# Kernel tuning notes

Hardware: AMD Instinct MI355X
Metric: run time of the kernel (lower is better)

Reference implementation:

```python
import jax, jax.numpy as jnp
import numpy as np

L, P, D, AL = 48, 2048, 50, 5
ONEHOT = 5 * D + 5  # 255, leaf one-hot size per encode()


def setup_inputs() -> dict:
    rng = np.random.default_rng(0)
    # node types: 0=leaf 1=unary 2=exist 3=univ 4=binary 5=functor 6=predicate
    node_type = np.zeros((L, P), np.int64)
    node_type[1:] = rng.integers(0, 7, size=(L - 1, P))
    children = -np.ones((L, P, AL), np.int64)
    for l in range(1, L):
        hi = l * P  # children must come from earlier levels (topological order)
        nt = node_type[l]
        n_child = np.where(nt == 0, 0,
                  np.where(nt <= 3, 1,
                  np.where(nt == 4, 2, rng.integers(1, AL + 1, size=P))))
        samp = rng.integers(0, hi, size=(P, AL))
        m = np.arange(AL)[None, :] < n_child[:, None]
        children[l] = np.where(m, samp, -1)
    # two-hot leaf encoding per encode(): v[category]=1 (0..4) and v[i+5]=1
    cat = rng.integers(0, 5, size=(L, P))
    ident = rng.integers(0, 5 * D, size=(L, P))
    onehot = np.zeros((L, P, ONEHOT), np.float32)
    li, pi = np.meshgrid(np.arange(L), np.arange(P), indexing='ij')
    onehot[li, pi, ident + 5] = 1.0
    onehot[li, pi, cat] = 1.0

    def lin(i, out_d, in_d):
        k = jax.random.fold_in(jax.random.key(0), i)
        kw, kb = jax.random.split(k)
        W = jax.random.normal(kw, (out_d, in_d), jnp.float32) * (in_d ** -0.5)
        b = jax.random.normal(kb, (out_d,), jnp.float32) * 0.01
        return W, b

    W_leaf, b_leaf = lin(0, D, ONEHOT)
    W_unary, b_unary = lin(1, D, D)
    W_exist, b_exist = lin(2, D, D)
    W_univ, b_univ = lin(3, D, D)
    W_bin, b_bin = lin(4, D, 3 * D)
    W_fun, b_fun = lin(5, D, (1 + AL) * D)
    W_pred, b_pred = lin(6, D, (1 + AL) * D)
    W_final, b_final = lin(7, ONEHOT, D)
    return dict(node_type=jnp.asarray(node_type, jnp.int32),
                children=jnp.asarray(children, jnp.int32),
                onehot=jnp.asarray(onehot),
                W_leaf=W_leaf, b_leaf=b_leaf, W_unary=W_unary, b_unary=b_unary,
                W_exist=W_exist, b_exist=b_exist, W_univ=W_univ, b_univ=b_univ,
                W_bin=W_bin, b_bin=b_bin, W_fun=W_fun, b_fun=b_fun,
                W_pred=W_pred, b_pred=b_pred, W_final=W_final, b_final=b_final)


def reference(node_type, children, onehot,
              W_leaf, b_leaf, W_unary, b_unary, W_exist, b_exist,
              W_univ, b_univ, W_bin, b_bin, W_fun, b_fun,
              W_pred, b_pred, W_final, b_final):
    relu = jax.nn.relu

    def step(buf, xs):
        l, nt, ch, oh = xs  # nt:[P], ch:[P,AL], oh:[P,ONEHOT]
        leaf = relu(oh @ W_leaf.T + b_leaf)                      # relu(leaf_net(onehot))
        mask = (ch >= 0).astype(buf.dtype)[..., None]
        ce = buf[jnp.clip(ch, 0)] * mask                          # [P,AL,D] child embeddings
        c0, c1 = ce[:, 0], ce[:, 1]
        unary = relu(c0 @ W_unary.T + b_unary)
        exist = relu(c0 @ W_exist.T + b_exist)
        univ = relu(c0 @ W_univ.T + b_univ)
        binv = relu(jnp.concatenate([c0, leaf, c1], -1) @ W_bin.T + b_bin)  # cat[left, op, right]
        fin = jnp.concatenate([leaf, ce.reshape(P, AL * D)], -1)  # [P,(1+AL)*D]
        fun = relu(fin @ W_fun.T + b_fun)
        pred = relu(fin @ W_pred.T + b_pred)
        outs = jnp.stack([leaf, unary, exist, univ, binv, fun, pred])  # [7,P,D]
        out = jnp.take_along_axis(outs, nt[None, :, None], axis=0)[0]
        buf = jax.lax.dynamic_update_slice(buf, out, (l * P, 0))
        return buf, None

    buf0 = jnp.zeros((L * P, D), onehot.dtype)
    xs = (jnp.arange(L), node_type, children, onehot)
    buf, _ = jax.lax.scan(step, buf0, xs)
    root = buf[-1]
    return root @ W_final.T + b_final  # self.final(self.visit(input)), shape [255]
```

## Files before the change

### kernel.cpp

```cpp
#include <hip/hip_runtime.h>

#define L_ 48
#define P_ 2048
#define D_ 50
#define AL_ 5
#define OH_ 255
#define NNODES (L_*P_)
#define MAXN_ 256
#define HSZ 1024
#define NTHREADS 512
#define NWAVES 8

__device__ __forceinline__ float dot50(const float* __restrict__ W, const float* in) {
    float a0 = 0.f, a1 = 0.f, a2 = 0.f, a3 = 0.f;
    #pragma unroll
    for (int j = 0; j < 48; j += 4) {
        float2 w0 = *reinterpret_cast<const float2*>(W + j);
        float2 w1 = *reinterpret_cast<const float2*>(W + j + 2);
        a0 += w0.x * in[j];
        a1 += w0.y * in[j + 1];
        a2 += w1.x * in[j + 2];
        a3 += w1.y * in[j + 3];
    }
    float2 wl = *reinterpret_cast<const float2*>(W + 48);
    a0 += wl.x * in[48];
    a1 += wl.y * in[49];
    return (a0 + a1) + (a2 + a3);
}

__device__ __forceinline__ float dotrow(const float* __restrict__ W, const float* in, int len) {
    float a0 = 0.f, a1 = 0.f, a2 = 0.f, a3 = 0.f;
    int j = 0;
    for (; j + 4 <= len; j += 4) {
        a0 += W[j] * in[j]; a1 += W[j+1] * in[j+1];
        a2 += W[j+2] * in[j+2]; a3 += W[j+3] * in[j+3];
    }
    for (; j < len; ++j) a0 += W[j] * in[j];
    return (a0 + a1) + (a2 + a3);
}

__device__ __forceinline__ float pf4(const float* __restrict__ p, int n, int t, int nth) {
    float s = 0.f;
    for (int i = t * 4; i + 3 < n; i += nth * 4) {
        float4 v = *reinterpret_cast<const float4*>(p + i);
        s += v.x + v.y + v.z + v.w;
    }
    return s;
}

__global__ __launch_bounds__(NTHREADS)
void formula_kernel(const int* __restrict__ node_type,
                    const int* __restrict__ children,
                    const float* __restrict__ onehot,
                    const float* __restrict__ W_leaf,  const float* __restrict__ b_leaf,
                    const float* __restrict__ W_unary, const float* __restrict__ b_unary,
                    const float* __restrict__ W_exist, const float* __restrict__ b_exist,
                    const float* __restrict__ W_univ,  const float* __restrict__ b_univ,
                    const float* __restrict__ W_bin,   const float* __restrict__ b_bin,
                    const float* __restrict__ W_fun,   const float* __restrict__ b_fun,
                    const float* __restrict__ W_pred,  const float* __restrict__ b_pred,
                    const float* __restrict__ W_final, const float* __restrict__ b_final,
                    float* __restrict__ out)
{
    __shared__ int h_key[HSZ];
    __shared__ int h_val[HSZ];
    __shared__ int list[MAXN_];
    __shared__ int nt_l[MAXN_];
    __shared__ int dep[MAXN_];
    __shared__ int order[MAXN_];
    __shared__ int ch_l[MAXN_][AL_];
    __shared__ int dcnt[48], doff[48], dfill[48];
    __shared__ int cnt_sh, maxd_sh;
    __shared__ float emb_s[MAXN_][D_];
    __shared__ float leaf_s[MAXN_][D_];
    __shared__ int   nzj[NWAVES][16];
    __shared__ float nzv[NWAVES][16];

    const int tid  = threadIdx.x;
    const int lane = tid & 63;
    const int wave = tid >> 6;
    volatile int* vcnt = &cnt_sh;

    if (wave == 0) {
        for (int i = lane; i < HSZ; i += 64) h_key[i] = -1;
        __builtin_amdgcn_wave_barrier();
        if (lane == 0) {
            cnt_sh = 1;
            list[0] = NNODES - 1;
            unsigned h = ((unsigned)(NNODES - 1) * 2654435761u) >> 16;
            for (;;) { int i = (int)(h & (HSZ - 1));
                       if (h_key[i] == -1) { h_key[i] = NNODES - 1; h_val[i] = 0; break; } ++h; }
        }
        __builtin_amdgcn_wave_barrier();

        int fs = 0, fe = 1;
        for (int round = 0; round < 48 && fs < fe; ++round) {
            const int npairs = (fe - fs) * AL_;
            for (int base = 0; base < npairs; base += 256) {
                const int m = (npairs - base < 256) ? (npairs - base) : 256;
                int cv[4];
                #pragma unroll
                for (int u = 0; u < 4; ++u) {
                    int t = base + lane + u * 64;
                    cv[u] = (t < base + m)
                        ? children[(size_t)list[fs + t / AL_] * AL_ + (t % AL_)] : -1;
                }
                #pragma unroll
                for (int u = 0; u < 4; ++u) {
                    int c = cv[u];
                    if (c >= 0) {
                        unsigned h = ((unsigned)c * 2654435761u) >> 16;
                        for (;;) {
                            int i = (int)(h & (HSZ - 1));
                            int prev = atomicCAS(&h_key[i], -1, c);
                            if (prev == -1) {
                                int pos = atomicAdd(&cnt_sh, 1);
                                h_val[i] = pos;
                                if (pos < MAXN_) list[pos] = c;
                                break;
                            }
                            if (prev == c) break;
                            ++h;
                        }
                    }
                }
            }
            __builtin_amdgcn_wave_barrier();
            fs = fe;
            int c2 = *vcnt;
            fe = c2 < MAXN_ ? c2 : MAXN_;
            __builtin_amdgcn_wave_barrier();
        }

        const int count = (*vcnt < MAXN_) ? *vcnt : MAXN_;

        for (int t = lane; t < count * 6; t += 64) {
            int i = t / 6, j = t % 6;
            int n = list[i];
            if (j == 0) {
                nt_l[i] = node_type[n];
            } else {
                int c = children[(size_t)n * AL_ + (j - 1)];
                int sl = -1;
                if (c >= 0) {
                    unsigned h = ((unsigned)c * 2654435761u) >> 16;
                    for (;;) {
                        int ii = (int)(h & (HSZ - 1));
                        if (h_key[ii] == c) { sl = h_val[ii]; break; }
                        ++h;
                    }
                    if (sl >= MAXN_) sl = -1;
                }
                ch_l[i][j - 1] = sl;
            }
        }
    } else {
        const int t = tid - 64, nth = NTHREADS - 64;
        float s = 0.f;
        s += pf4(W_leaf,  D_ * OH_,    t, nth);
        s += pf4(W_unary, D_ * D_,     t, nth);
        s += pf4(W_exist, D_ * D_,     t, nth);
        s += pf4(W_univ,  D_ * D_,     t, nth);
        s += pf4(W_bin,   D_ * 3 * D_, t, nth);
        s += pf4(W_fun,   D_ * 6 * D_, t, nth);
        s += pf4(W_pred,  D_ * 6 * D_, t, nth);
        s += pf4(W_final, OH_ * D_,    t, nth);
        if (t < 64) {
            s += b_leaf[t % D_] + b_unary[t % D_] + b_exist[t % D_] + b_univ[t % D_]
               + b_bin[t % D_] + b_fun[t % D_] + b_pred[t % D_] + b_final[t];
        }
        asm volatile("" :: "v"(s));
    }
    __syncthreads();

    const int count = (cnt_sh < MAXN_) ? cnt_sh : MAXN_;

    if (wave == 0) {
        volatile int* vdep = dep;
        for (int i = lane; i < count; i += 64) vdep[i] = 0;
        __builtin_amdgcn_wave_barrier();
        for (int it = 0; it < 48; ++it) {
            bool anych = false;
            for (int i = lane; i < count; i += 64) {
                int d = 0;
                #pragma unroll
                for (int k = 0; k < AL_; ++k) {
                    int cs = ch_l[i][k];
                    if (cs >= 0) { int dd = vdep[cs] + 1; if (dd > d) d = dd; }
                }
                if (d > vdep[i]) { vdep[i] = d; anych = true; }
            }
            __builtin_amdgcn_wave_barrier();
            if (!__any(anych)) break;
        }
        for (int i = lane; i < 48; i += 64) { dcnt[i] = 0; dfill[i] = 0; }
        __builtin_amdgcn_wave_barrier();
        for (int i = lane; i < count; i += 64) atomicAdd(&dcnt[dep[i]], 1);
        __builtin_amdgcn_wave_barrier();
        {
            int v = (lane < 48) ? dcnt[lane] : 0;
            int incl = v;
            #pragma unroll
            for (int dlt = 1; dlt < 64; dlt <<= 1) {
                int o = __shfl_up(incl, dlt);
                if (lane >= dlt) incl += o;
            }
            if (lane < 48) doff[lane] = incl - v;
            unsigned long long b = __ballot(lane < 48 && v != 0);
            if (lane == 0) maxd_sh = 63 - __builtin_clzll(b);
        }
        __builtin_amdgcn_wave_barrier();
        for (int i = lane; i < count; i += 64) {
            int d = dep[i];
            int pos = doff[d] + atomicAdd(&dfill[d], 1);
            order[pos] = i;
        }
    } else {
        for (int slot = wave - 1; slot < count; slot += NWAVES - 1) {
            const int nt = nt_l[slot];
            if (nt >= 1 && nt <= 3) continue;
            const int n = list[slot];
            const float* oh = onehot + (size_t)n * OH_;
            float v[4]; int c2 = 0;
            #pragma unroll
            for (int t = 0; t < 4; ++t) {
                int j = lane * 4 + t;
                v[t] = (j < OH_) ? oh[j] : 0.0f;
                if (v[t] != 0.0f) c2++;
            }
            int incl = c2;
            #pragma unroll
            for (int dlt = 1; dlt < 64; dlt <<= 1) {
                int o = __shfl_up(incl, dlt);
                if (lane >= dlt) incl += o;
            }
            const int excl = incl - c2;
            const int total = __shfl(incl, 63);
            if (total <= 16) {
                int pos = excl;
                #pragma unroll
                for (int t = 0; t < 4; ++t)
                    if (v[t] != 0.0f) { nzj[wave][pos] = lane * 4 + t; nzv[wave][pos] = v[t]; pos++; }
            }
            __builtin_amdgcn_wave_barrier();
            if (lane < D_) {
                float sacc = b_leaf[lane];
                if (total <= 16) {
                    for (int i2 = 0; i2 < total; ++i2)
                        sacc += nzv[wave][i2] * W_leaf[lane * OH_ + nzj[wave][i2]];
                } else {
                    sacc += dotrow(W_leaf + lane * OH_, oh, OH_);
                }
                float lv = fmaxf(sacc, 0.0f);
                if (nt == 0) emb_s[slot][lane] = lv;
                else         leaf_s[slot][lane] = lv;
            }
            __builtin_amdgcn_wave_barrier();
        }
    }
    __syncthreads();

    const int maxd = maxd_sh;

    for (int d = 1; d <= maxd; ++d) {
        const int s0 = doff[d], cn = dcnt[d];
        for (int jj = wave; jj < cn; jj += NWAVES) {
            const int slot = order[s0 + jj];
            const int nt = nt_l[slot];
            if (lane < D_) {
                float s;
                if (nt <= 3) {
                    const float* W = (nt == 1) ? W_unary : (nt == 2) ? W_exist : W_univ;
                    const float* b = (nt == 1) ? b_unary : (nt == 2) ? b_exist : b_univ;
                    s = b[lane];
                    const int cs0 = ch_l[slot][0];
                    if (cs0 >= 0) s += dot50(W + lane * D_, emb_s[cs0]);
                } else if (nt == 4) {
                    const float* W = W_bin + lane * 3 * D_;
                    s = b_bin[lane];
                    const int cs0 = ch_l[slot][0], cs1 = ch_l[slot][1];
                    if (cs0 >= 0) s += dot50(W, emb_s[cs0]);
                    s += dot50(W + D_, leaf_s[slot]);
                    if (cs1 >= 0) s += dot50(W + 2 * D_, emb_s[cs1]);
                } else {
                    const float* W = ((nt == 5) ? W_fun : W_pred) + lane * 6 * D_;
                    s = ((nt == 5) ? b_fun : b_pred)[lane] + dot50(W, leaf_s[slot]);
                    #pragma unroll
                    for (int k = 0; k < AL_; ++k) {
                        int cs = ch_l[slot][k];
                        if (cs >= 0) s += dot50(W + (1 + k) * D_, emb_s[cs]);
                    }
                }
                emb_s[slot][lane] = fmaxf(s, 0.0f);
            }
        }
        __syncthreads();
    }

    for (int o = tid; o < OH_; o += NTHREADS)
        out[o] = b_final[o] + dot50(W_final + o * D_, emb_s[0]);
}

extern "C" void kernel_launch(void* const* d_in, const int* in_sizes, int n_in,
                              void* d_out, int out_size, void* d_ws, size_t ws_size,
                              hipStream_t stream) {
    const int*   node_type = (const int*)d_in[0];
    const int*   children  = (const int*)d_in[1];
    const float* onehot    = (const float*)d_in[2];
    const float* W_leaf  = (const float*)d_in[3];  const float* b_leaf  = (const float*)d_in[4];
    const float* W_unary = (const float*)d_in[5];  const float* b_unary = (const float*)d_in[6];
    const float* W_exist = (const float*)d_in[7];  const float* b_exist = (const float*)d_in[8];
    const float* W_univ  = (const float*)d_in[9];  const float* b_univ  = (const float*)d_in[10];
    const float* W_bin   = (const float*)d_in[11]; const float* b_bin   = (const float*)d_in[12];
    const float* W_fun   = (const float*)d_in[13]; const float* b_fun   = (const float*)d_in[14];
    const float* W_pred  = (const float*)d_in[15]; const float* b_pred  = (const float*)d_in[16];
    const float* W_final = (const float*)d_in[17]; const float* b_final = (const float*)d_in[18];

    float* out = (float*)d_out;

    formula_kernel<<<1, NTHREADS, 0, stream>>>(
        node_type, children, onehot,
        W_leaf, b_leaf, W_unary, b_unary, W_exist, b_exist, W_univ, b_univ,
        W_bin, b_bin, W_fun, b_fun, W_pred, b_pred, W_final, b_final,
        out);
}
```

Baseline: 23.40 us.

## Replace depth-level barriers with ready-flag dataflow over index-sorted nodes

Drops the per-depth dependency computation and level-by-level __syncthreads schedule. Nodes are instead sorted by global index, which is already a topological order, and waves spin on per-node LDS ready flags before consuming child embeddings. The change also prefetches each discovered node's children, type and onehot rows into LDS scratch during BFS, fuses the leaf computation into the main loop, and pads embedding rows for float4 LDS reads. The spin-waiting adds a risk of stalls and depends on fence ordering, and the rank sort is quadratic in the node count.

```diff
diff --git a/kernel.cpp b/kernel.cpp
--- a/kernel.cpp
+++ b/kernel.cpp
@@ -10,21 +10,29 @@
 #define HSZ 1024
 #define NTHREADS 512
 #define NWAVES 8
-
-__device__ __forceinline__ float dot50(const float* __restrict__ W, const float* in) {
+#define SPIN_BOUND (1 << 24)
+
+__device__ __forceinline__ void pfl(const void* g, void* lds_scratch) {
+    __builtin_amdgcn_global_load_lds(
+        (const __attribute__((address_space(1))) unsigned int*)g,
+        (__attribute__((address_space(3))) unsigned int*)lds_scratch,
+        4, 0, 0);
+}
+
+__device__ __forceinline__ float dot50L(const float* __restrict__ Wg, const float* inL) {
+    const float4* x4 = (const float4*)inL;
     float a0 = 0.f, a1 = 0.f, a2 = 0.f, a3 = 0.f;
     #pragma unroll
-    for (int j = 0; j < 48; j += 4) {
-        float2 w0 = *reinterpret_cast<const float2*>(W + j);
-        float2 w1 = *reinterpret_cast<const float2*>(W + j + 2);
-        a0 += w0.x * in[j];
-        a1 += w0.y * in[j + 1];
-        a2 += w1.x * in[j + 2];
-        a3 += w1.y * in[j + 3];
-    }
-    float2 wl = *reinterpret_cast<const float2*>(W + 48);
-    a0 += wl.x * in[48];
-    a1 += wl.y * in[49];
+    for (int q = 0; q < 12; ++q) {
+        float4 x = x4[q];
+        float2 w0 = *(const float2*)(Wg + q * 4);
+        float2 w1 = *(const float2*)(Wg + q * 4 + 2);
+        a0 += w0.x * x.x; a1 += w0.y * x.y;
+        a2 += w1.x * x.z; a3 += w1.y * x.w;
+    }
+    float4 xt = x4[12];
+    float2 wt = *(const float2*)(Wg + 48);
+    a0 += wt.x * xt.x; a1 += wt.y * xt.y;
     return (a0 + a1) + (a2 + a3);
 }
 
@@ -66,36 +74,43 @@
     __shared__ int h_val[HSZ];
     __shared__ int list[MAXN_];
     __shared__ int nt_l[MAXN_];
-    __shared__ int dep[MAXN_];
     __shared__ int order[MAXN_];
+    __shared__ int rdy[MAXN_];
     __shared__ int ch_l[MAXN_][AL_];
-    __shared__ int dcnt[48], doff[48], dfill[48];
-    __shared__ int cnt_sh, maxd_sh;
-    __shared__ float emb_s[MAXN_][D_];
-    __shared__ float leaf_s[MAXN_][D_];
+    __shared__ int cnt_sh;
+    __shared__ __align__(16) float emb_s[MAXN_][52];
+    __shared__ __align__(16) float lrow[NWAVES][52];
     __shared__ int   nzj[NWAVES][16];
     __shared__ float nzv[NWAVES][16];
+    __shared__ unsigned pfscr[64];
 
     const int tid  = threadIdx.x;
     const int lane = tid & 63;
     const int wave = tid >> 6;
-    volatile int* vcnt = &cnt_sh;
 
     if (wave == 0) {
         for (int i = lane; i < HSZ; i += 64) h_key[i] = -1;
         __builtin_amdgcn_wave_barrier();
         if (lane == 0) {
             cnt_sh = 1;
-            list[0] = NNODES - 1;
-            unsigned h = ((unsigned)(NNODES - 1) * 2654435761u) >> 16;
+            const int root = NNODES - 1;
+            list[0] = root;
+            unsigned h = ((unsigned)root * 2654435761u) >> 16;
             for (;;) { int i = (int)(h & (HSZ - 1));
-                       if (h_key[i] == -1) { h_key[i] = NNODES - 1; h_val[i] = 0; break; } ++h; }
+                       if (h_key[i] == -1) { h_key[i] = root; h_val[i] = 0; break; } ++h; }
+            pfl(&node_type[root], pfscr);
+            const char* ohb = (const char*)(onehot + (size_t)root * OH_);
+            #pragma unroll
+            for (int q = 0; q < 16; ++q) pfl(ohb + q * 64, pfscr);
+            pfl(ohb + 1016, pfscr);
         }
         __builtin_amdgcn_wave_barrier();
 
+        int total_reg = 1;
         int fs = 0, fe = 1;
         for (int round = 0; round < 48 && fs < fe; ++round) {
             const int npairs = (fe - fs) * AL_;
+            int ic = 0;
             for (int base = 0; base < npairs; base += 256) {
                 const int m = (npairs - base < 256) ? (npairs - base) : 256;
                 int cv[4];
@@ -117,6 +132,14 @@
                                 int pos = atomicAdd(&cnt_sh, 1);
                                 h_val[i] = pos;
                                 if (pos < MAXN_) list[pos] = c;
+                                ic++;
+                                const char* chb = (const char*)&children[(size_t)c * AL_];
+                                pfl(chb, pfscr); pfl(chb + 16, pfscr);
+                                pfl(&node_type[c], pfscr);
+                                const char* ohb = (const char*)(onehot + (size_t)c * OH_);
+                                #pragma unroll
+                                for (int q = 0; q < 16; ++q) pfl(ohb + q * 64, pfscr);
+                                pfl(ohb + 1016, pfscr);
                                 break;
                             }
                             if (prev == c) break;
@@ -126,33 +149,13 @@
                 }
             }
             __builtin_amdgcn_wave_barrier();
+            int tot = ic;
+            #pragma unroll
+            for (int d = 1; d < 64; d <<= 1) tot += __shfl_xor(tot, d);
+            total_reg += tot;
             fs = fe;
-            int c2 = *vcnt;
-            fe = c2 < MAXN_ ? c2 : MAXN_;
+            fe = (total_reg < MAXN_) ? total_reg : MAXN_;
             __builtin_amdgcn_wave_barrier();
-        }
-
-        const int count = (*vcnt < MAXN_) ? *vcnt : MAXN_;
-
-        for (int t = lane; t < count * 6; t += 64) {
-            int i = t / 6, j = t % 6;
-            int n = list[i];
-            if (j == 0) {
-                nt_l[i] = node_type[n];
-            } else {
-                int c = children[(size_t)n * AL_ + (j - 1)];
-                int sl = -1;
-                if (c >= 0) {
-                    unsigned h = ((unsigned)c * 2654435761u) >> 16;
-                    for (;;) {
-                        int ii = (int)(h & (HSZ - 1));
-                        if (h_key[ii] == c) { sl = h_val[ii]; break; }
-                        ++h;
-                    }
-                    if (sl >= MAXN_) sl = -1;
-                }
-                ch_l[i][j - 1] = sl;
-            }
         }
     } else {
         const int t = tid - 64, nth = NTHREADS - 64;
@@ -175,51 +178,43 @@
 
     const int count = (cnt_sh < MAXN_) ? cnt_sh : MAXN_;
 
-    if (wave == 0) {
-        volatile int* vdep = dep;
-        for (int i = lane; i < count; i += 64) vdep[i] = 0;
-        __builtin_amdgcn_wave_barrier();
-        for (int it = 0; it < 48; ++it) {
-            bool anych = false;
-            for (int i = lane; i < count; i += 64) {
-                int d = 0;
-                #pragma unroll
-                for (int k = 0; k < AL_; ++k) {
-                    int cs = ch_l[i][k];
-                    if (cs >= 0) { int dd = vdep[cs] + 1; if (dd > d) d = dd; }
-                }
-                if (d > vdep[i]) { vdep[i] = d; anych = true; }
-            }
-            __builtin_amdgcn_wave_barrier();
-            if (!__any(anych)) break;
-        }
-        for (int i = lane; i < 48; i += 64) { dcnt[i] = 0; dfill[i] = 0; }
-        __builtin_amdgcn_wave_barrier();
-        for (int i = lane; i < count; i += 64) atomicAdd(&dcnt[dep[i]], 1);
-        __builtin_amdgcn_wave_barrier();
-        {
-            int v = (lane < 48) ? dcnt[lane] : 0;
-            int incl = v;
-            #pragma unroll
-            for (int dlt = 1; dlt < 64; dlt <<= 1) {
-                int o = __shfl_up(incl, dlt);
-                if (lane >= dlt) incl += o;
-            }
-            if (lane < 48) doff[lane] = incl - v;
-            unsigned long long b = __ballot(lane < 48 && v != 0);
-            if (lane == 0) maxd_sh = 63 - __builtin_clzll(b);
-        }
-        __builtin_amdgcn_wave_barrier();
-        for (int i = lane; i < count; i += 64) {
-            int d = dep[i];
-            int pos = doff[d] + atomicAdd(&dfill[d], 1);
-            order[pos] = i;
-        }
-    } else {
-        for (int slot = wave - 1; slot < count; slot += NWAVES - 1) {
-            const int nt = nt_l[slot];
-            if (nt >= 1 && nt <= 3) continue;
-            const int n = list[slot];
+    for (int t = tid; t < count * 6; t += NTHREADS) {
+        int i = t / 6, j = t % 6;
+        int n = list[i];
+        if (j == 0) {
+            nt_l[i] = node_type[n];
+        } else {
+            int c = children[(size_t)n * AL_ + (j - 1)];
+            int sl = -1;
+            if (c >= 0) {
+                unsigned h = ((unsigned)c * 2654435761u) >> 16;
+                for (;;) {
+                    int ii = (int)(h & (HSZ - 1));
+                    if (h_key[ii] == c) { sl = h_val[ii]; break; }
+                    ++h;
+                }
+                if (sl >= MAXN_) sl = -1;
+            }
+            ch_l[i][j - 1] = sl;
+        }
+    }
+    for (int i = tid; i < count; i += NTHREADS) {
+        int me = list[i];
+        int r = 0;
+        for (int j = 0; j < count; ++j) r += (list[j] < me);
+        order[r] = i;
+        rdy[i] = 0;
+    }
+    __syncthreads();
+
+    volatile int* vrdy = rdy;
+    for (int pos = wave; pos < count; pos += NWAVES) {
+        const int slot = order[pos];
+        const int nt = nt_l[slot];
+        const int n = list[slot];
+
+        float leafv = 0.0f;
+        if (nt == 0 || nt >= 4) {
             const float* oh = onehot + (size_t)n * OH_;
             float v[4]; int c2 = 0;
             #pragma unroll
@@ -237,10 +232,10 @@
             const int excl = incl - c2;
             const int total = __shfl(incl, 63);
             if (total <= 16) {
-                int pos = excl;
+                int p2 = excl;
                 #pragma unroll
                 for (int t = 0; t < 4; ++t)
-                    if (v[t] != 0.0f) { nzj[wave][pos] = lane * 4 + t; nzv[wave][pos] = v[t]; pos++; }
+                    if (v[t] != 0.0f) { nzj[wave][p2] = lane * 4 + t; nzv[wave][p2] = v[t]; p2++; }
             }
             __builtin_amdgcn_wave_barrier();
             if (lane < D_) {
@@ -251,22 +246,28 @@
                 } else {
                     sacc += dotrow(W_leaf + lane * OH_, oh, OH_);
                 }
-                float lv = fmaxf(sacc, 0.0f);
-                if (nt == 0) emb_s[slot][lane] = lv;
-                else         leaf_s[slot][lane] = lv;
+                leafv = fmaxf(sacc, 0.0f);
+                if (nt >= 4) lrow[wave][lane] = leafv;
             }
             __builtin_amdgcn_wave_barrier();
         }
-    }
-    __syncthreads();
-
-    const int maxd = maxd_sh;
-
-    for (int d = 1; d <= maxd; ++d) {
-        const int s0 = doff[d], cn = dcnt[d];
-        for (int jj = wave; jj < cn; jj += NWAVES) {
-            const int slot = order[s0 + jj];
-            const int nt = nt_l[slot];
+
+        float outv = 0.0f;
+        if (nt == 0) {
+            outv = leafv;
+        } else {
+            #pragma unroll
+            for (int k = 0; k < AL_; ++k) {
+                int cs = ch_l[slot][k];
+                if (cs >= 0) {
+                    int guard = 0;
+                    while (vrdy[cs] == 0 && guard < SPIN_BOUND) {
+                        __builtin_amdgcn_s_sleep(1);
+                        ++guard;
+                    }
+                }
+            }
+            __threadfence_block();
             if (lane < D_) {
                 float s;
                 if (nt <= 3) {
@@ -274,31 +275,35 @@
                     const float* b = (nt == 1) ? b_unary : (nt == 2) ? b_exist : b_univ;
                     s = b[lane];
                     const int cs0 = ch_l[slot][0];
-                    if (cs0 >= 0) s += dot50(W + lane * D_, emb_s[cs0]);
+                    if (cs0 >= 0) s += dot50L(W + lane * D_, emb_s[cs0]);
                 } else if (nt == 4) {
                     const float* W = W_bin + lane * 3 * D_;
                     s = b_bin[lane];
                     const int cs0 = ch_l[slot][0], cs1 = ch_l[slot][1];
-                    if (cs0 >= 0) s += dot50(W, emb_s[cs0]);
-                    s += dot50(W + D_, leaf_s[slot]);
-                    if (cs1 >= 0) s += dot50(W + 2 * D_, emb_s[cs1]);
+                    if (cs0 >= 0) s += dot50L(W, emb_s[cs0]);
+                    s += dot50L(W + D_, lrow[wave]);
+                    if (cs1 >= 0) s += dot50L(W + 2 * D_, emb_s[cs1]);
                 } else {
                     const float* W = ((nt == 5) ? W_fun : W_pred) + lane * 6 * D_;
-                    s = ((nt == 5) ? b_fun : b_pred)[lane] + dot50(W, leaf_s[slot]);
+                    s = ((nt == 5) ? b_fun : b_pred)[lane] + dot50L(W, lrow[wave]);
                     #pragma unroll
                     for (int k = 0; k < AL_; ++k) {
                         int cs = ch_l[slot][k];
-                        if (cs >= 0) s += dot50(W + (1 + k) * D_, emb_s[cs]);
+                        if (cs >= 0) s += dot50L(W + (1 + k) * D_, emb_s[cs]);
                     }
                 }
-                emb_s[slot][lane] = fmaxf(s, 0.0f);
-            }
-        }
-        __syncthreads();
-    }
-
+                outv = fmaxf(s, 0.0f);
+            }
+        }
+        if (lane < D_) emb_s[slot][lane] = outv;
+        __threadfence_block();
+        if (lane == 0) vrdy[slot] = 1;
+    }
+    __syncthreads();
+
+    const int rootslot = order[count - 1];
     for (int o = tid; o < OH_; o += NTHREADS)
-        out[o] = b_final[o] + dot50(W_final + o * D_, emb_s[0]);
+        out[o] = b_final[o] + dot50L(W_final + o * D_, emb_s[rootslot]);
 }
 
 extern "C" void kernel_launch(void* const* d_in, const int* in_sizes, int n_in,
```

After: 26.48 us. +13.1%, slower.
